# Optimization experiments

Hardware: AMD Instinct MI355X
Metric: run time of the kernel (lower is better)

The kernel has to match this reference:

```python
import jax, jax.numpy as jnp
import numpy as np

THRESHOLD = 1.0
DECAY = 0.9


def setup_inputs() -> dict:
    key = jax.random.key(0)
    ks = jax.random.split(key, 7)
    B, D_in, H, D_out = 512, 1024, 2048, 1024
    return {
        "x": jax.random.normal(ks[0], (B, D_in), dtype=jnp.float32),
        "W0": jax.random.normal(ks[1], (H, D_in), dtype=jnp.float32) * 0.03,
        "b0": jax.random.normal(ks[2], (H,), dtype=jnp.float32) * 0.03,
        "W1": jax.random.normal(ks[3], (H, H), dtype=jnp.float32) * 0.03,
        "b1": jax.random.normal(ks[4], (H,), dtype=jnp.float32) * 0.03,
        "W2": jax.random.normal(ks[5], (D_out, H), dtype=jnp.float32) * 0.03,
        "b2": jax.random.normal(ks[6], (D_out,), dtype=jnp.float32) * 0.03,
        "time_steps": 50,
    }


def _lif_layer(layer_input, W, b, time_steps):
    # layer_input is constant over time in the original module, so the
    # per-neuron Linear is computed ONCE as a single matmul.
    I = layer_input @ W.T + b  # [B, out_dim] input current, fixed per step
    V0 = jnp.zeros_like(I)

    def step(V, _):
        V = V * DECAY + I
        s = (V > THRESHOLD).astype(I.dtype)
        V = V * (1.0 - s)
        return V, s

    _, spikes = jax.lax.scan(step, V0, None, length=time_steps)  # [T, B, out]
    spikes = jnp.transpose(spikes, (1, 2, 0))  # [B, out, T]
    return spikes


def reference(x, W0, b0, W1, b1, W2, b2, time_steps):
    s0 = _lif_layer(x, W0, b0, time_steps)
    s1 = _lif_layer(s0.mean(axis=2), W1, b1, time_steps)
    s2 = _lif_layer(s1.mean(axis=2), W2, b2, time_steps)
    # matches (layer_outputs[-1], all_spikes)
    return (s2, s0, s1, s2)
```

## Files before the change

### kernel.cpp

```cpp
#include <hip/hip_runtime.h>

typedef unsigned long long u64;
typedef unsigned int u32;

constexpr int TPB = 256;
constexpr int BM = 64, BN = 64, BK = 64;
constexpr int T  = 50;
constexpr int M  = 512;

template<bool IN_MASK>
__global__ __launch_bounds__(TPB)
void gemm_part(const void* __restrict__ Ain, const int K, const int N,
               const float* __restrict__ W, float* __restrict__ pp)
{
    __shared__ float sA[BK][BM + 4];
    __shared__ float sB[BK][BN + 4];

    const int tid = threadIdx.x;
    const int tx  = tid & 15;
    const int ty  = tid >> 4;
    const int n0  = blockIdx.x * BN;
    const int m0  = blockIdx.y * BM;
    const int kbase = blockIdx.z * 512;

    const int lr  = tid >> 2;
    const int klc = (tid & 3) << 4;

    float S[4][4];
    #pragma unroll
    for (int i = 0; i < 4; ++i)
        #pragma unroll
        for (int j = 0; j < 4; ++j) S[i][j] = 0.0f;

    const float* aF = (const float*)Ain + (size_t)(m0 + lr) * K + kbase + klc;
    const u64*   aM = (const u64*)Ain   + (size_t)(m0 + lr) * K + kbase + klc;
    const float* wp = W + (size_t)(n0 + lr) * K + kbase + klc;

    float4 fa[4]; uint4 ma[8]; float4 fw[4];

    auto loadA = [&](int k0) {
        if constexpr (IN_MASK) {
            const uint4* p = reinterpret_cast<const uint4*>(aM + k0);
            #pragma unroll
            for (int c = 0; c < 8; ++c) ma[c] = p[c];
        } else {
            #pragma unroll
            for (int c = 0; c < 4; ++c)
                fa[c] = *reinterpret_cast<const float4*>(aF + k0 + 4 * c);
        }
    };
    auto loadW = [&](int k0) {
        #pragma unroll
        for (int c = 0; c < 4; ++c)
            fw[c] = *reinterpret_cast<const float4*>(wp + k0 + 4 * c);
    };

    constexpr int NT = 512 / BK;
    loadA(0); loadW(0);

    for (int t = 0; t < NT; ++t) {
        __syncthreads();
        if constexpr (IN_MASK) {
            #pragma unroll
            for (int i = 0; i < 16; ++i) {
                const u32 lo = (i & 1) ? ma[i >> 1].z : ma[i >> 1].x;
                const u32 hi = (i & 1) ? ma[i >> 1].w : ma[i >> 1].y;
                sA[klc + i][lr] = __fdiv_rn((float)(__popc(lo) + __popc(hi)), 50.0f);
            }
        } else {
            #pragma unroll
            for (int c = 0; c < 4; ++c) {
                sA[klc + 4 * c + 0][lr] = fa[c].x;
                sA[klc + 4 * c + 1][lr] = fa[c].y;
                sA[klc + 4 * c + 2][lr] = fa[c].z;
                sA[klc + 4 * c + 3][lr] = fa[c].w;
            }
        }
        #pragma unroll
        for (int c = 0; c < 4; ++c) {
            sB[klc + 4 * c + 0][lr] = fw[c].x;
            sB[klc + 4 * c + 1][lr] = fw[c].y;
            sB[klc + 4 * c + 2][lr] = fw[c].z;
            sB[klc + 4 * c + 3][lr] = fw[c].w;
        }
        __syncthreads();

        if (t + 1 < NT) { loadA((t + 1) * BK); loadW((t + 1) * BK); }

        #pragma unroll
        for (int kk = 0; kk < BK; ++kk) {
            const float4 a4 = *reinterpret_cast<const float4*>(&sA[kk][ty * 4]);
            const float4 b4 = *reinterpret_cast<const float4*>(&sB[kk][tx * 4]);
            const float a[4] = {a4.x, a4.y, a4.z, a4.w};
            const float b[4] = {b4.x, b4.y, b4.z, b4.w};
            #pragma unroll
            for (int i = 0; i < 4; ++i)
                #pragma unroll
                for (int j = 0; j < 4; ++j)
                    S[i][j] = __fmaf_rn(a[i], b[j], S[i][j]);
        }
    }

    float* dst = pp + (size_t)blockIdx.z * M * N;
    #pragma unroll
    for (int i = 0; i < 4; ++i)
        #pragma unroll
        for (int j = 0; j < 4; ++j)
            dst[(size_t)(m0 + ty * 4 + i) * N + (n0 + tx * 4 + j)] = S[i][j];
}

template<bool DUP, bool WMASK>
__global__ __launch_bounds__(TPB)
void merge_lif_expand(const float* __restrict__ pp, const int nchain,
                      const int N, const float* __restrict__ bias,
                      u64* __restrict__ maskOut, float* __restrict__ out,
                      float* __restrict__ dup)
{
    __shared__ u64 lm[TPB];
    const int tid = threadIdx.x;
    const size_t base = (size_t)blockIdx.x * TPB;
    const size_t idx  = base + tid;
    const size_t cs   = (size_t)M * N;

    float s = pp[idx];
    for (int c = 1; c < nchain; ++c) s = __fadd_rn(s, pp[(size_t)c * cs + idx]);
    const float I = __fadd_rn(s, bias[idx & (size_t)(N - 1)]);

    float V = 0.0f; u64 msk = 0ull;
    #pragma unroll 1
    for (int t = 0; t < T; ++t) {
        V = __fadd_rn(__fmul_rn(V, 0.9f), I);
        if (V > 1.0f) { V = 0.0f; msk |= (1ull << t); }
    }
    if constexpr (WMASK) maskOut[idx] = msk;
    lm[tid] = msk;
    __syncthreads();

    constexpr int TOTQ = TPB * T / 4;
    for (int q4 = tid; q4 < TOTQ; q4 += TPB) {
        const int q = q4 << 2;
        int nn = q / T;
        int tt = q - nn * T;
        u64 mk = lm[nn];
        float vals[4];
        #pragma unroll
        for (int c = 0; c < 4; ++c) {
            if (tt >= T) { tt -= T; ++nn; mk = lm[nn]; }
            vals[c] = (float)((mk >> tt) & 1ull);
            ++tt;
        }
        const float4 v4 = make_float4(vals[0], vals[1], vals[2], vals[3]);
        const size_t off = base * T + q;
        *reinterpret_cast<float4*>(out + off) = v4;
        if constexpr (DUP) *reinterpret_cast<float4*>(dup + off) = v4;
    }
}

template<bool IN_MASK>
__global__ __launch_bounds__(TPB)
void lif_gemm_mask(const void* __restrict__ Ain, const int K, const int N,
                   const float* __restrict__ W, const float* __restrict__ bias,
                   u64* __restrict__ maskOut)
{
    __shared__ float sA[BK][BM + 4];
    __shared__ float sB[BK][BN + 4];
    const int tid = threadIdx.x;
    const int tx = tid & 15, ty = tid >> 4;
    const int n0 = blockIdx.x * BN, m0 = blockIdx.y * BM;
    const int lr = tid >> 2, klc = (tid & 3) << 4;

    float S[4][4], Ia[4][4];
    #pragma unroll
    for (int i = 0; i < 4; ++i)
        #pragma unroll
        for (int j = 0; j < 4; ++j) { S[i][j] = 0.0f; Ia[i][j] = 0.0f; }

    const float* aF = (const float*)Ain + (size_t)(m0 + lr) * K + klc;
    const u64*   aM = (const u64*)Ain   + (size_t)(m0 + lr) * K + klc;
    const float* wp = W + (size_t)(n0 + lr) * K + klc;
    float4 fa[4]; uint4 ma[8]; float4 fw[4];

    auto loadA = [&](int k0) {
        if constexpr (IN_MASK) {
            const uint4* p = reinterpret_cast<const uint4*>(aM + k0);
            #pragma unroll
            for (int c = 0; c < 8; ++c) ma[c] = p[c];
        } else {
            #pragma unroll
            for (int c = 0; c < 4; ++c)
                fa[c] = *reinterpret_cast<const float4*>(aF + k0 + 4 * c);
        }
    };
    auto loadW = [&](int k0) {
        #pragma unroll
        for (int c = 0; c < 4; ++c)
            fw[c] = *reinterpret_cast<const float4*>(wp + k0 + 4 * c);
    };

    const int NT = K / BK;
    loadA(0); loadW(0);
    for (int t = 0; t < NT; ++t) {
        __syncthreads();
        if constexpr (IN_MASK) {
            #pragma unroll
            for (int i = 0; i < 16; ++i) {
                const u32 lo = (i & 1) ? ma[i >> 1].z : ma[i >> 1].x;
                const u32 hi = (i & 1) ? ma[i >> 1].w : ma[i >> 1].y;
                sA[klc + i][lr] = __fdiv_rn((float)(__popc(lo) + __popc(hi)), 50.0f);
            }
        } else {
            #pragma unroll
            for (int c = 0; c < 4; ++c) {
                sA[klc + 4 * c + 0][lr] = fa[c].x;
                sA[klc + 4 * c + 1][lr] = fa[c].y;
                sA[klc + 4 * c + 2][lr] = fa[c].z;
                sA[klc + 4 * c + 3][lr] = fa[c].w;
            }
        }
        #pragma unroll
        for (int c = 0; c < 4; ++c) {
            sB[klc + 4 * c + 0][lr] = fw[c].x;
            sB[klc + 4 * c + 1][lr] = fw[c].y;
            sB[klc + 4 * c + 2][lr] = fw[c].z;
            sB[klc + 4 * c + 3][lr] = fw[c].w;
        }
        __syncthreads();
        if (t + 1 < NT) { loadA((t + 1) * BK); loadW((t + 1) * BK); }
        #pragma unroll
        for (int kk = 0; kk < BK; ++kk) {
            const float4 a4 = *reinterpret_cast<const float4*>(&sA[kk][ty * 4]);
            const float4 b4 = *reinterpret_cast<const float4*>(&sB[kk][tx * 4]);
            const float a[4] = {a4.x, a4.y, a4.z, a4.w};
            const float b[4] = {b4.x, b4.y, b4.z, b4.w};
            #pragma unroll
            for (int i = 0; i < 4; ++i)
                #pragma unroll
                for (int j = 0; j < 4; ++j)
                    S[i][j] = __fmaf_rn(a[i], b[j], S[i][j]);
        }
        if ((((t + 1) * BK) & 511) == 0) {
            #pragma unroll
            for (int i = 0; i < 4; ++i)
                #pragma unroll
                for (int j = 0; j < 4; ++j) {
                    Ia[i][j] = __fadd_rn(Ia[i][j], S[i][j]);
                    S[i][j]  = 0.0f;
                }
        }
    }
    #pragma unroll
    for (int i = 0; i < 4; ++i)
        #pragma unroll
        for (int j = 0; j < 4; ++j) {
            const int mi = ty * 4 + i, nj = tx * 4 + j;
            const float I = __fadd_rn(Ia[i][j], bias[n0 + nj]);
            float V = 0.0f; u64 msk = 0ull;
            #pragma unroll 1
            for (int t = 0; t < T; ++t) {
                V = __fadd_rn(__fmul_rn(V, 0.9f), I);
                if (V > 1.0f) { V = 0.0f; msk |= (1ull << t); }
            }
            maskOut[(size_t)(m0 + mi) * N + (n0 + nj)] = msk;
        }
}

template<bool DUP>
__global__ __launch_bounds__(TPB)
void expand_spikes(const u64* __restrict__ mask, float* __restrict__ out,
                   float* __restrict__ dup)
{
    __shared__ u64 lm[TPB];
    const int tid = threadIdx.x;
    const size_t base = (size_t)blockIdx.x * TPB;
    lm[tid] = mask[base + tid];
    __syncthreads();
    constexpr int TOTQ = TPB * T / 4;
    for (int q4 = tid; q4 < TOTQ; q4 += TPB) {
        const int q = q4 << 2;
        int nn = q / T, tt = q - nn * T;
        u64 mk = lm[nn];
        float vals[4];
        #pragma unroll
        for (int c = 0; c < 4; ++c) {
            if (tt >= T) { tt -= T; ++nn; mk = lm[nn]; }
            vals[c] = (float)((mk >> tt) & 1ull);
            ++tt;
        }
        const float4 v4 = make_float4(vals[0], vals[1], vals[2], vals[3]);
        const size_t off = base * T + q;
        *reinterpret_cast<float4*>(out + off) = v4;
        if constexpr (DUP) *reinterpret_cast<float4*>(dup + off) = v4;
    }
}

__global__ __launch_bounds__(TPB)
void copy_f4(const float* __restrict__ src, float* __restrict__ dst, int nquads)
{
    int i = blockIdx.x * blockDim.x + threadIdx.x;
    int stride = gridDim.x * blockDim.x;
    for (; i < nquads; i += stride)
        reinterpret_cast<float4*>(dst)[i] = reinterpret_cast<const float4*>(src)[i];
}

extern "C" void kernel_launch(void* const* d_in, const int* in_sizes, int n_in,
                              void* d_out, int out_size, void* d_ws, size_t ws_size,
                              hipStream_t stream) {
    const float* x  = (const float*)d_in[0];
    const float* W0 = (const float*)d_in[1];
    const float* b0 = (const float*)d_in[2];
    const float* W1 = (const float*)d_in[3];
    const float* b1 = (const float*)d_in[4];
    const float* W2 = (const float*)d_in[5];
    const float* b2 = (const float*)d_in[6];
    float* out = (float*)d_out;

    constexpr int H = 2048, DOUT = 1024;
    const size_t s2sz = (size_t)M * DOUT * T;
    const size_t s0sz = (size_t)M * H * T;
    const size_t NH = (size_t)M * H;
    const size_t ND = (size_t)M * DOUT;

    float* s2a = out;
    float* s0  = out + s2sz;
    float* s1  = s0 + s0sz;
    float* s2b = s1 + s0sz;

    dim3 blk(TPB);
    const size_t WS_NEED = (2 * NH + 4 * NH + 4 * ND) * sizeof(float)
                         + (NH + NH) * sizeof(u64);

    if (ws_size >= WS_NEED) {
        float* pp0 = (float*)d_ws;
        float* pp1 = pp0 + 2 * NH;
        float* pp2 = pp1 + 4 * NH;
        u64* mask0 = (u64*)(pp2 + 4 * ND);
        u64* mask1 = mask0 + NH;

        gemm_part<false><<<dim3(H / BN, M / BM, 2), blk, 0, stream>>>(
            x, 1024, H, W0, pp0);
        merge_lif_expand<false, true><<<(int)(NH / TPB), blk, 0, stream>>>(
            pp0, 2, H, b0, mask0, s0, nullptr);
        gemm_part<true><<<dim3(H / BN, M / BM, 4), blk, 0, stream>>>(
            mask0, H, H, W1, pp1);
        merge_lif_expand<false, true><<<(int)(NH / TPB), blk, 0, stream>>>(
            pp1, 4, H, b1, mask1, s1, nullptr);
        gemm_part<true><<<dim3(DOUT / BN, M / BM, 4), blk, 0, stream>>>(
            mask1, H, DOUT, W2, pp2);
        merge_lif_expand<true, false><<<(int)(ND / TPB), blk, 0, stream>>>(
            pp2, 4, DOUT, b2, nullptr, s2b, s2a);
    } else if (ws_size >= ND * sizeof(u64)) {
        u64* mask0 = (u64*)s1;
        u64* mask1 = (u64*)s2a;
        u64* mask2 = (u64*)d_ws;
        dim3 gH(H / BN, M / BM), gD(DOUT / BN, M / BM);
        lif_gemm_mask<false><<<gH, blk, 0, stream>>>(x, 1024, H, W0, b0, mask0);
        lif_gemm_mask<true ><<<gH, blk, 0, stream>>>(mask0, H, H, W1, b1, mask1);
        lif_gemm_mask<true ><<<gD, blk, 0, stream>>>(mask1, H, DOUT, W2, b2, mask2);
        expand_spikes<false><<<(int)(NH / TPB), blk, 0, stream>>>(mask0, s0, nullptr);
        expand_spikes<false><<<(int)(NH / TPB), blk, 0, stream>>>(mask1, s1, nullptr);
        expand_spikes<true ><<<(int)(ND / TPB), blk, 0, stream>>>(mask2, s2b, s2a);
    } else {
        u64* mask0 = (u64*)s1;
        u64* mask1 = (u64*)s2a;
        dim3 gH(H / BN, M / BM), gD(DOUT / BN, M / BM);
        lif_gemm_mask<false><<<gH, blk, 0, stream>>>(x, 1024, H, W0, b0, mask0);
        lif_gemm_mask<true ><<<gH, blk, 0, stream>>>(mask0, H, H, W1, b1, mask1);
        expand_spikes<false><<<(int)(NH / TPB), blk, 0, stream>>>(mask0, s0, nullptr);
        u64* mask2 = (u64*)s0;
        lif_gemm_mask<true ><<<gD, blk, 0, stream>>>(mask1, H, DOUT, W2, b2, mask2);
        expand_spikes<false><<<(int)(NH / TPB), blk, 0, stream>>>(mask1, s1, nullptr);
        expand_spikes<true ><<<(int)(ND / TPB), blk, 0, stream>>>(mask2, s2b, s2a);
        lif_gemm_mask<false><<<dim3(H / BN, 1), blk, 0, stream>>>(x, 1024, H, W0, b0, (u64*)s2b);
        expand_spikes<false><<<(int)(NH / TPB / 8), blk, 0, stream>>>((u64*)s2b, s0, nullptr);
        lif_gemm_mask<true ><<<gD, blk, 0, stream>>>(mask1, H, DOUT, W2, b2, (u64*)s2a);
        expand_spikes<true ><<<(int)(ND / TPB), blk, 0, stream>>>((u64*)s2a, s2b, s2a);
    }
}
```

Measured before the change: 298.4 us.

## Use 128x64 GEMM tiles and pass float spike means between layers

The split-K GEMM tile grows from 64x64 to 128x64, with each thread now computing an 8x4 output block and storing it as float4. The merge kernel writes the per-neuron spike-rate mean as a float instead of a 64-bit mask, so the next GEMM loads plain floats and skips popcount and division on every A-tile load. Larger tiles raise reuse of W from shared memory but use more registers and launch half as many blocks. The lowest-workspace fallback path is removed.

```diff
diff --git a/kernel.cpp b/kernel.cpp
--- a/kernel.cpp
+++ b/kernel.cpp
@@ -4,55 +4,46 @@
 typedef unsigned int u32;
 
 constexpr int TPB = 256;
-constexpr int BM = 64, BN = 64, BK = 64;
 constexpr int T  = 50;
 constexpr int M  = 512;
 
-template<bool IN_MASK>
 __global__ __launch_bounds__(TPB)
-void gemm_part(const void* __restrict__ Ain, const int K, const int N,
+void gemm_part(const float* __restrict__ A, const int K, const int N,
                const float* __restrict__ W, float* __restrict__ pp)
 {
-    __shared__ float sA[BK][BM + 4];
-    __shared__ float sB[BK][BN + 4];
+    constexpr int BM2 = 128, BN2 = 64, BK = 64;
+    __shared__ float sA[BK][BM2 + 4];
+    __shared__ float sB[BK][BN2 + 4];
 
     const int tid = threadIdx.x;
     const int tx  = tid & 15;
     const int ty  = tid >> 4;
-    const int n0  = blockIdx.x * BN;
-    const int m0  = blockIdx.y * BM;
+    const int n0  = blockIdx.x * BN2;
+    const int m0  = blockIdx.y * BM2;
     const int kbase = blockIdx.z * 512;
 
-    const int lr  = tid >> 2;
-    const int klc = (tid & 3) << 4;
-
-    float S[4][4];
+    const int ar = tid >> 1, aks = (tid & 1) << 5;
+    const int wr = tid >> 2, wks = (tid & 3) << 4;
+
+    float S[8][4];
     #pragma unroll
-    for (int i = 0; i < 4; ++i)
+    for (int i = 0; i < 8; ++i)
         #pragma unroll
         for (int j = 0; j < 4; ++j) S[i][j] = 0.0f;
 
-    const float* aF = (const float*)Ain + (size_t)(m0 + lr) * K + kbase + klc;
-    const u64*   aM = (const u64*)Ain   + (size_t)(m0 + lr) * K + kbase + klc;
-    const float* wp = W + (size_t)(n0 + lr) * K + kbase + klc;
-
-    float4 fa[4]; uint4 ma[8]; float4 fw[4];
-
-    auto loadA = [&](int k0) {
-        if constexpr (IN_MASK) {
-            const uint4* p = reinterpret_cast<const uint4*>(aM + k0);
-            #pragma unroll
-            for (int c = 0; c < 8; ++c) ma[c] = p[c];
-        } else {
-            #pragma unroll
-            for (int c = 0; c < 4; ++c)
-                fa[c] = *reinterpret_cast<const float4*>(aF + k0 + 4 * c);
-        }
+    const float* aP = A + (size_t)(m0 + ar) * K + kbase + aks;
+    const float* wP = W + (size_t)(n0 + wr) * K + kbase + wks;
+
+    float4 fa[8], fw[4];
+    auto loadA = [&](int t) {
+        #pragma unroll
+        for (int c = 0; c < 8; ++c)
+            fa[c] = *reinterpret_cast<const float4*>(aP + t * BK + 4 * c);
     };
-    auto loadW = [&](int k0) {
+    auto loadW = [&](int t) {
         #pragma unroll
         for (int c = 0; c < 4; ++c)
-            fw[c] = *reinterpret_cast<const float4*>(wp + k0 + 4 * c);
+            fw[c] = *reinterpret_cast<const float4*>(wP + t * BK + 4 * c);
     };
 
     constexpr int NT = 512 / BK;
@@ -60,41 +51,33 @@
 
     for (int t = 0; t < NT; ++t) {
         __syncthreads();
-        if constexpr (IN_MASK) {
-            #pragma unroll
-            for (int i = 0; i < 16; ++i) {
-                const u32 lo = (i & 1) ? ma[i >> 1].z : ma[i >> 1].x;
-                const u32 hi = (i & 1) ? ma[i >> 1].w : ma[i >> 1].y;
-                sA[klc + i][lr] = __fdiv_rn((float)(__popc(lo) + __popc(hi)), 50.0f);
-            }
-        } else {
-            #pragma unroll
-            for (int c = 0; c < 4; ++c) {
-                sA[klc + 4 * c + 0][lr] = fa[c].x;
-                sA[klc + 4 * c + 1][lr] = fa[c].y;
-                sA[klc + 4 * c + 2][lr] = fa[c].z;
-                sA[klc + 4 * c + 3][lr] = fa[c].w;
-            }
+        #pragma unroll
+        for (int c = 0; c < 8; ++c) {
+            sA[aks + 4 * c + 0][ar] = fa[c].x;
+            sA[aks + 4 * c + 1][ar] = fa[c].y;
+            sA[aks + 4 * c + 2][ar] = fa[c].z;
+            sA[aks + 4 * c + 3][ar] = fa[c].w;
         }
         #pragma unroll
         for (int c = 0; c < 4; ++c) {
-            sB[klc + 4 * c + 0][lr] = fw[c].x;
-            sB[klc + 4 * c + 1][lr] = fw[c].y;
-            sB[klc + 4 * c + 2][lr] = fw[c].z;
-            sB[klc + 4 * c + 3][lr] = fw[c].w;
+            sB[wks + 4 * c + 0][wr] = fw[c].x;
+            sB[wks + 4 * c + 1][wr] = fw[c].y;
+            sB[wks + 4 * c + 2][wr] = fw[c].z;
+            sB[wks + 4 * c + 3][wr] = fw[c].w;
         }
         __syncthreads();
 
-        if (t + 1 < NT) { loadA((t + 1) * BK); loadW((t + 1) * BK); }
+        if (t + 1 < NT) { loadA(t + 1); loadW(t + 1); }
 
         #pragma unroll
         for (int kk = 0; kk < BK; ++kk) {
-            const float4 a4 = *reinterpret_cast<const float4*>(&sA[kk][ty * 4]);
+            const float4 a0 = *reinterpret_cast<const float4*>(&sA[kk][ty * 8]);
+            const float4 a1 = *reinterpret_cast<const float4*>(&sA[kk][ty * 8 + 4]);
             const float4 b4 = *reinterpret_cast<const float4*>(&sB[kk][tx * 4]);
-            const float a[4] = {a4.x, a4.y, a4.z, a4.w};
+            const float a[8] = {a0.x, a0.y, a0.z, a0.w, a1.x, a1.y, a1.z, a1.w};
             const float b[4] = {b4.x, b4.y, b4.z, b4.w};
             #pragma unroll
-            for (int i = 0; i < 4; ++i)
+            for (int i = 0; i < 8; ++i)
                 #pragma unroll
                 for (int j = 0; j < 4; ++j)
                     S[i][j] = __fmaf_rn(a[i], b[j], S[i][j]);
@@ -103,17 +86,18 @@
 
     float* dst = pp + (size_t)blockIdx.z * M * N;
     #pragma unroll
-    for (int i = 0; i < 4; ++i)
-        #pragma unroll
-        for (int j = 0; j < 4; ++j)
-            dst[(size_t)(m0 + ty * 4 + i) * N + (n0 + tx * 4 + j)] = S[i][j];
-}
-
-template<bool DUP, bool WMASK>
+    for (int i = 0; i < 8; ++i) {
+        const size_t off = (size_t)(m0 + ty * 8 + i) * N + (n0 + tx * 4);
+        *reinterpret_cast<float4*>(dst + off) =
+            make_float4(S[i][0], S[i][1], S[i][2], S[i][3]);
+    }
+}
+
+template<bool DUP, bool WMEAN>
 __global__ __launch_bounds__(TPB)
 void merge_lif_expand(const float* __restrict__ pp, const int nchain,
                       const int N, const float* __restrict__ bias,
-                      u64* __restrict__ maskOut, float* __restrict__ out,
+                      float* __restrict__ meanOut, float* __restrict__ out,
                       float* __restrict__ dup)
 {
     __shared__ u64 lm[TPB];
@@ -132,7 +116,8 @@
         V = __fadd_rn(__fmul_rn(V, 0.9f), I);
         if (V > 1.0f) { V = 0.0f; msk |= (1ull << t); }
     }
-    if constexpr (WMASK) maskOut[idx] = msk;
+    if constexpr (WMEAN)
+        meanOut[idx] = __fdiv_rn((float)__popcll(msk), 50.0f);
     lm[tid] = msk;
     __syncthreads();
 
@@ -162,6 +147,7 @@
                    const float* __restrict__ W, const float* __restrict__ bias,
                    u64* __restrict__ maskOut)
 {
+    constexpr int BM = 64, BN = 64, BK = 64;
     __shared__ float sA[BK][BM + 4];
     __shared__ float sB[BK][BN + 4];
     const int tid = threadIdx.x;
@@ -293,15 +279,6 @@
     }
 }
 
-__global__ __launch_bounds__(TPB)
-void copy_f4(const float* __restrict__ src, float* __restrict__ dst, int nquads)
-{
-    int i = blockIdx.x * blockDim.x + threadIdx.x;
-    int stride = gridDim.x * blockDim.x;
-    for (; i < nquads; i += stride)
-        reinterpret_cast<float4*>(dst)[i] = reinterpret_cast<const float4*>(src)[i];
-}
-
 extern "C" void kernel_launch(void* const* d_in, const int* in_sizes, int n_in,
                               void* d_out, int out_size, void* d_ws, size_t ws_size,
                               hipStream_t stream) {
@@ -326,53 +303,37 @@
     float* s2b = s1 + s0sz;
 
     dim3 blk(TPB);
-    const size_t WS_NEED = (2 * NH + 4 * NH + 4 * ND) * sizeof(float)
-                         + (NH + NH) * sizeof(u64);
+    const size_t WS_NEED = (2 * NH + 4 * NH + 4 * ND + 2 * NH) * sizeof(float);
 
     if (ws_size >= WS_NEED) {
-        float* pp0 = (float*)d_ws;
-        float* pp1 = pp0 + 2 * NH;
-        float* pp2 = pp1 + 4 * NH;
-        u64* mask0 = (u64*)(pp2 + 4 * ND);
-        u64* mask1 = mask0 + NH;
-
-        gemm_part<false><<<dim3(H / BN, M / BM, 2), blk, 0, stream>>>(
+        float* pp0   = (float*)d_ws;
+        float* pp1   = pp0 + 2 * NH;
+        float* pp2   = pp1 + 4 * NH;
+        float* mean0 = pp2 + 4 * ND;
+        float* mean1 = mean0 + NH;
+
+        gemm_part<<<dim3(H / 64, M / 128, 2), blk, 0, stream>>>(
             x, 1024, H, W0, pp0);
         merge_lif_expand<false, true><<<(int)(NH / TPB), blk, 0, stream>>>(
-            pp0, 2, H, b0, mask0, s0, nullptr);
-        gemm_part<true><<<dim3(H / BN, M / BM, 4), blk, 0, stream>>>(
-            mask0, H, H, W1, pp1);
+            pp0, 2, H, b0, mean0, s0, nullptr);
+        gemm_part<<<dim3(H / 64, M / 128, 4), blk, 0, stream>>>(
+            mean0, H, H, W1, pp1);
         merge_lif_expand<false, true><<<(int)(NH / TPB), blk, 0, stream>>>(
-            pp1, 4, H, b1, mask1, s1, nullptr);
-        gemm_part<true><<<dim3(DOUT / BN, M / BM, 4), blk, 0, stream>>>(
-            mask1, H, DOUT, W2, pp2);
+            pp1, 4, H, b1, mean1, s1, nullptr);
+        gemm_part<<<dim3(DOUT / 64, M / 128, 4), blk, 0, stream>>>(
+            mean1, H, DOUT, W2, pp2);
         merge_lif_expand<true, false><<<(int)(ND / TPB), blk, 0, stream>>>(
             pp2, 4, DOUT, b2, nullptr, s2b, s2a);
-    } else if (ws_size >= ND * sizeof(u64)) {
+    } else {
         u64* mask0 = (u64*)s1;
         u64* mask1 = (u64*)s2a;
         u64* mask2 = (u64*)d_ws;
-        dim3 gH(H / BN, M / BM), gD(DOUT / BN, M / BM);
+        dim3 gH(H / 64, M / 64), gD(DOUT / 64, M / 64);
         lif_gemm_mask<false><<<gH, blk, 0, stream>>>(x, 1024, H, W0, b0, mask0);
         lif_gemm_mask<true ><<<gH, blk, 0, stream>>>(mask0, H, H, W1, b1, mask1);
         lif_gemm_mask<true ><<<gD, blk, 0, stream>>>(mask1, H, DOUT, W2, b2, mask2);
         expand_spikes<false><<<(int)(NH / TPB), blk, 0, stream>>>(mask0, s0, nullptr);
         expand_spikes<false><<<(int)(NH / TPB), blk, 0, stream>>>(mask1, s1, nullptr);
         expand_spikes<true ><<<(int)(ND / TPB), blk, 0, stream>>>(mask2, s2b, s2a);
-    } else {
-        u64* mask0 = (u64*)s1;
-        u64* mask1 = (u64*)s2a;
-        dim3 gH(H / BN, M / BM), gD(DOUT / BN, M / BM);
-        lif_gemm_mask<false><<<gH, blk, 0, stream>>>(x, 1024, H, W0, b0, mask0);
-        lif_gemm_mask<true ><<<gH, blk, 0, stream>>>(mask0, H, H, W1, b1, mask1);
-        expand_spikes<false><<<(int)(NH / TPB), blk, 0, stream>>>(mask0, s0, nullptr);
-        u64* mask2 = (u64*)s0;
-        lif_gemm_mask<true ><<<gD, blk, 0, stream>>>(mask1, H, DOUT, W2, b2, mask2);
-        expand_spikes<false><<<(int)(NH / TPB), blk, 0, stream>>>(mask1, s1, nullptr);
-        expand_spikes<true ><<<(int)(ND / TPB), blk, 0, stream>>>(mask2, s2b, s2a);
-        lif_gemm_mask<false><<<dim3(H / BN, 1), blk, 0, stream>>>(x, 1024, H, W0, b0, (u64*)s2b);
-        expand_spikes<false><<<(int)(NH / TPB / 8), blk, 0, stream>>>((u64*)s2b, s0, nullptr);
-        lif_gemm_mask<true ><<<gD, blk, 0, stream>>>(mask1, H, DOUT, W2, b2, (u64*)s2a);
-        expand_spikes<true ><<<(int)(ND / TPB), blk, 0, stream>>>((u64*)s2a, s2b, s2a);
-    }
-}
+    }
+}
```

New measurement: 267.1 us. 10.5% less time.
